# Kernel optimization log

Hardware: AMD Instinct MI355X
Metric: run time of the kernel (lower is better)

## Reference

```python
import jax, jax.numpy as jnp
import numpy as np

B, S, D, H = 2, 2048, 2048, 16
DH = D // H  # 128
EPS = 1e-6


def _rms_norm(x, w):
    # RMSNorm over last dim with learnable scale
    var = jnp.mean(jnp.square(x), axis=-1, keepdims=True)
    return x * jax.lax.rsqrt(var + EPS) * w


def _apply_rope(x, angles):
    # x: [B, S, H, DH]; angles: [S, DH//2]; interleaved pair rotation
    xs = x.reshape(*x.shape[:-1], DH // 2, 2)
    x0, x1 = xs[..., 0], xs[..., 1]
    cos = jnp.cos(angles)[None, :, None, :]  # [1,S,1,DH/2]
    sin = jnp.sin(angles)[None, :, None, :]
    r0 = x0 * cos - x1 * sin
    r1 = x0 * sin + x1 * cos
    return jnp.stack([r0, r1], axis=-1).reshape(x.shape)


def setup_inputs() -> dict:
    key = jax.random.key(0)
    ks = jax.random.split(key, 4)
    x = jax.random.normal(ks[0], (B, S, D), dtype=jnp.float32)
    # standard RoPE angle table: pos * inv_freq
    inv_freq = 1.0 / (10000.0 ** (jnp.arange(0, DH, 2, dtype=jnp.float32) / DH))
    pos = jnp.arange(S, dtype=jnp.float32)
    rp_freqs = pos[:, None] * inv_freq[None, :]  # [S, DH/2]
    Win = jax.random.normal(ks[1], (3 * D, D), dtype=jnp.float32) * (D ** -0.5)
    b_in = jnp.zeros((3 * D,), dtype=jnp.float32)
    Wout = jax.random.normal(ks[2], (D, D), dtype=jnp.float32) * (D ** -0.5)
    b_out = jnp.zeros((D,), dtype=jnp.float32)
    qk_w = jnp.ones((DH,), dtype=jnp.float32)
    out_w = jnp.ones((D,), dtype=jnp.float32)
    return {"x": x, "rp_freqs": rp_freqs, "Win": Win, "b_in": b_in,
            "Wout": Wout, "b_out": b_out, "qk_w": qk_w, "out_w": out_w}


def reference(x, rp_freqs, Win, b_in, Wout, b_out, qk_w, out_w):
    b, s, d = x.shape
    qkv = jnp.einsum('bsd,ed->bse', x, Win) + b_in  # [B,S,3D]
    qkv = qkv.reshape(b, s, 3, H, DH)
    q, k, v = qkv[:, :, 0], qkv[:, :, 1], qkv[:, :, 2]  # each [B,S,H,DH]
    q = _apply_rope(q, rp_freqs)
    k = _apply_rope(k, rp_freqs)
    q = _rms_norm(q, qk_w)
    k = _rms_norm(k, qk_w)
    # causal SDPA, scale = 1/sqrt(DH) (default)
    a = jax.nn.dot_product_attention(q, k, v, is_causal=True)  # [B,S,H,DH]
    a = a.reshape(b, s, d)
    a = _rms_norm(a, out_w)
    return jnp.einsum('bsd,ed->bse', a, Wout) + b_out
```

## Files before the change

### kernel.cpp

```cpp
#include <hip/hip_runtime.h>
#include <cstdint>
#include <cstddef>

#define Bq  2
#define Sq  2048
#define Dq  2048
#define Hq  16
#define DHq 128
#define E3q 6144

typedef __attribute__((ext_vector_type(8))) short s16x8;
typedef __attribute__((ext_vector_type(4))) float f32x4;

__device__ __forceinline__ unsigned short f2bf(float f){
  union { float f; unsigned u; } v; v.f = f;
  unsigned r = v.u + 0x7FFFu + ((v.u >> 16) & 1u);
  return (unsigned short)(r >> 16);
}
__device__ __forceinline__ float bf2f(unsigned short b){
  union { unsigned u; float f; } v; v.u = ((unsigned)b) << 16;
  return v.f;
}
__device__ __forceinline__ unsigned cvtpk_bf16(float lo, float hi){
  unsigned r;
  asm("v_cvt_pk_bf16_f32 %0, %1, %2" : "=v"(r) : "v"(lo), "v"(hi));
  return r;
}

__device__ __forceinline__ void gload_lds16(const void* g, void* l){
  __builtin_amdgcn_global_load_lds(
      (const __attribute__((address_space(1))) void*)g,
      (__attribute__((address_space(3))) void*)l, 16, 0, 0);
}

__global__ __launch_bounds__(256) void k_convert(const float* __restrict__ in,
                                                 unsigned short* __restrict__ out, int n4){
  int stride = gridDim.x * blockDim.x;
  for (int i = blockIdx.x*blockDim.x + threadIdx.x; i < n4; i += stride){
    float4 v = reinterpret_cast<const float4*>(in)[i];
    ushort4 o;
    o.x = f2bf(v.x); o.y = f2bf(v.y); o.z = f2bf(v.z); o.w = f2bf(v.w);
    reinterpret_cast<ushort4*>(out)[i] = o;
  }
}

template<int F32OUT>
__global__ __launch_bounds__(256, 2) void k_gemm_bt(const unsigned short* __restrict__ A,
                                                    const unsigned short* __restrict__ Bt,
                                                    const float* __restrict__ bias,
                                                    void* __restrict__ C,
                                                    int M, int N, int K){
  const int bid = blockIdx.x;
  const int xcd = bid & 7, u = bid >> 3;
  const int by = xcd*4 + (u & 3);
  const int bx = u >> 2;
  const int m0 = by * 128, n0 = bx * 256;

  const int tid = threadIdx.x;
  const int w = tid >> 6, lane = tid & 63, g = lane >> 4, c = lane & 15;

  __shared__ __align__(16) unsigned short L[3 * 12288];

  const int NT = K >> 5;

  const int r0 = tid >> 2, pc = tid & 3;
  const unsigned short* Ab0 = &A [(size_t)(m0 + r0      )*K + (size_t)((pc ^ (((r0      )>>1)&3))*8)];
  const unsigned short* Ab1 = &A [(size_t)(m0 + r0 +  64)*K + (size_t)((pc ^ (((r0 + 64)>>1)&3))*8)];
  const unsigned short* Bb0 = &Bt[(size_t)(n0 + r0      )*K + (size_t)((pc ^ (((r0      )>>1)&3))*8)];
  const unsigned short* Bb1 = &Bt[(size_t)(n0 + r0 +  64)*K + (size_t)((pc ^ (((r0 + 64)>>1)&3))*8)];
  const unsigned short* Bb2 = &Bt[(size_t)(n0 + r0 + 128)*K + (size_t)((pc ^ (((r0 +128)>>1)&3))*8)];
  const unsigned short* Bb3 = &Bt[(size_t)(n0 + r0 + 192)*K + (size_t)((pc ^ (((r0 +192)>>1)&3))*8)];

  auto stage = [&](int tile, int slot){
    const int kt = tile << 5;
    unsigned short* Ls = &L[slot * 12288];
    gload_lds16(Ab0 + kt, &Ls[tid*8]);
    gload_lds16(Ab1 + kt, &Ls[(tid+256)*8]);
    gload_lds16(Bb0 + kt, &Ls[4096 + tid*8]);
    gload_lds16(Bb1 + kt, &Ls[4096 + (tid+256)*8]);
    gload_lds16(Bb2 + kt, &Ls[4096 + (tid+512)*8]);
    gload_lds16(Bb3 + kt, &Ls[4096 + (tid+768)*8]);
  };

  f32x4 acc[8][4];
#pragma unroll
  for (int i=0;i<8;i++)
#pragma unroll
    for (int j=0;j<4;j++)
#pragma unroll
      for (int r=0;r<4;r++) acc[i][j][r] = 0.f;

  int aoff[8], boff[4];
#pragma unroll
  for (int mi=0;mi<8;mi++){
    int row = mi*16 + c;
    aoff[mi] = row*32 + ((g ^ ((row>>1)&3)) << 3);
  }
#pragma unroll
  for (int ni=0;ni<4;ni++){
    int row = w*64 + ni*16 + c;
    boff[ni] = 4096 + row*32 + ((g ^ ((row>>1)&3)) << 3);
  }

  stage(0,0); stage(1,1);

  int slot = 0;
  for (int t = 0; t < NT; ++t){
    if (t < NT-1) asm volatile("s_waitcnt vmcnt(6)" ::: "memory");
    else          asm volatile("s_waitcnt vmcnt(0)" ::: "memory");
    __builtin_amdgcn_s_barrier();
    __builtin_amdgcn_sched_barrier(0);
    if (t+2 < NT) stage(t+2, slot == 0 ? 2 : slot-1);

    const unsigned short* Ls = &L[slot * 12288];
    s16x8 bfr[4];
#pragma unroll
    for (int ni=0;ni<4;ni++) bfr[ni] = *(const s16x8*)&Ls[boff[ni]];
    __builtin_amdgcn_s_setprio(1);
#pragma unroll
    for (int mi=0;mi<8;mi++){
      s16x8 af = *(const s16x8*)&Ls[aoff[mi]];
#pragma unroll
      for (int ni=0;ni<4;ni++)
        acc[mi][ni] = __builtin_amdgcn_mfma_f32_16x16x32_bf16(af, bfr[ni], acc[mi][ni], 0,0,0);
    }
    __builtin_amdgcn_s_setprio(0);
    slot = (slot == 2) ? 0 : slot+1;
  }

#pragma unroll
  for (int ni=0;ni<4;ni++){
    const int col = n0 + w*64 + ni*16 + c;
    const float bv = bias[col];
#pragma unroll
    for (int mi=0;mi<8;mi++){
      const int row = m0 + mi*16 + g*4;
#pragma unroll
      for (int r=0;r<4;r++){
        float v = acc[mi][ni][r] + bv;
        if (F32OUT) ((float*)C)[(size_t)(row+r)*N + col] = v;
        else ((unsigned short*)C)[(size_t)(row+r)*N + col] = f2bf(v);
      }
    }
  }
}

__global__ __launch_bounds__(256) void k_rope_qk(const unsigned short* __restrict__ QKV,
                                                 const float* __restrict__ rp,
                                                 const float* __restrict__ qk_w,
                                                 unsigned short* __restrict__ Qp,
                                                 unsigned short* __restrict__ Kp){
  const int p = threadIdx.x;
  const int s = blockIdx.x*4 + threadIdx.y;
  const int h = blockIdx.y;
  const int b = blockIdx.z;
  const size_t n = (size_t)b*Sq + s;
  const int bh = b*Hq + h;

  float ang = rp[s*64 + p];
  float sn, cs; sincosf(ang, &sn, &cs);
  float w0 = qk_w[2*p], w1 = qk_w[2*p+1];
  const float QSCALE = 0.08838834764831845f * 1.4426950408889634f;

  {
    unsigned q01 = *(const unsigned*)&QKV[n*E3q + h*DHq + 2*p];
    float x0 = bf2f((unsigned short)(q01 & 0xFFFFu));
    float x1 = bf2f((unsigned short)(q01 >> 16));
    float r0 = x0*cs - x1*sn, r1 = x0*sn + x1*cs;
    float ss = r0*r0 + r1*r1;
#pragma unroll
    for (int m=1;m<64;m<<=1) ss += __shfl_xor(ss, m);
    float sc = rsqrtf(ss/128.f + 1e-6f) * QSCALE;
    unsigned short o0 = f2bf(r0*sc*w0), o1 = f2bf(r1*sc*w1);
    *(unsigned*)&Qp[((size_t)bh*Sq + s)*DHq + 2*p] = (unsigned)o0 | ((unsigned)o1<<16);
  }
  {
    unsigned k01 = *(const unsigned*)&QKV[n*E3q + Dq + h*DHq + 2*p];
    float x0 = bf2f((unsigned short)(k01 & 0xFFFFu));
    float x1 = bf2f((unsigned short)(k01 >> 16));
    float r0 = x0*cs - x1*sn, r1 = x0*sn + x1*cs;
    float ss = r0*r0 + r1*r1;
#pragma unroll
    for (int m=1;m<64;m<<=1) ss += __shfl_xor(ss, m);
    float sc = rsqrtf(ss/128.f + 1e-6f);
    unsigned short o0 = f2bf(r0*sc*w0), o1 = f2bf(r1*sc*w1);
    *(unsigned*)&Kp[((size_t)bh*Sq + s)*DHq + 2*p] = (unsigned)o0 | ((unsigned)o1<<16);
  }
}

__global__ __launch_bounds__(256) void k_transpose_v(const unsigned short* __restrict__ QKV,
                                                     unsigned short* __restrict__ Vt){
  const int sblk = blockIdx.x;
  const int bh = blockIdx.y;
  const int b = bh >> 4, h = bh & 15;
  const int tid = threadIdx.x;
  __shared__ unsigned short T[128][136];

  const size_t base = ((size_t)(b*Sq) + sblk*128) * E3q + 2*(size_t)Dq + h*DHq;
#pragma unroll
  for (int i=0;i<8;i++){
    int pk = tid + i*256;
    int row = pk >> 4, cc = (pk & 15) * 8;
    s16x8 v = *(const s16x8*)&QKV[base + (size_t)row*E3q + cc];
    *(s16x8*)&T[row][cc] = v;
  }
  __syncthreads();
  const int dh = tid >> 1, sh = (tid & 1) * 64;
  unsigned short buf[64];
#pragma unroll
  for (int s=0;s<64;s++) buf[s] = T[sh + s][dh];
  size_t obase = ((size_t)bh*DHq + dh)*Sq + sblk*128 + sh;
#pragma unroll
  for (int i=0;i<8;i++)
    *(s16x8*)&Vt[obase + i*8] = *(const s16x8*)&buf[i*8];
}

__global__ __launch_bounds__(256, 2) void k_attn(const unsigned short* __restrict__ Qp,
                                                 const unsigned short* __restrict__ Kp,
                                                 const unsigned short* __restrict__ Vt,
                                                 unsigned short* __restrict__ Ar){
  const int L = blockIdx.x;
  int bh, qtile;
  if (L < 256){ bh = L >> 3; qtile = 8 + (L & 7); }
  else { int Ml = L - 256; bh = Ml >> 3; qtile = 7 - (Ml & 7); }
  const int b = bh >> 4, h = bh & 15;
  const int tid = threadIdx.x;
  const int w = tid >> 6, lane = tid & 63, g = lane >> 4, c = lane & 15;
  const int r0w = qtile*128 + w*32;

  const unsigned short* Qh = Qp + (size_t)bh * Sq * DHq;
  const unsigned short* Kh = Kp + (size_t)bh * Sq * DHq;
  const unsigned short* Vh = Vt + (size_t)bh * DHq * Sq;

  __shared__ __align__(16) unsigned short Ks[2][64*128];
  __shared__ __align__(16) unsigned short Vs[2][128*64];
  __shared__ __align__(16) unsigned short Pl[4][32*64];
  unsigned short* Pw = &Pl[w][0];

  s16x8 qf[2][4];
#pragma unroll
  for (int mi=0;mi<2;mi++)
#pragma unroll
    for (int kc=0;kc<4;kc++)
      qf[mi][kc] = *(const s16x8*)&Qh[(size_t)(r0w + mi*16 + c)*DHq + kc*32 + g*8];

  f32x4 acc[2][8];
#pragma unroll
  for (int mi=0;mi<2;mi++)
#pragma unroll
    for (int dt=0;dt<8;dt++)
#pragma unroll
      for (int r=0;r<4;r++) acc[mi][dt][r] = 0.f;
  float m_r[2] = { -INFINITY, -INFINITY };
  float l_p[2] = { 0.f, 0.f };

  const int nsteps = 2*qtile + 2;

  auto stage = [&](int j0s, int bufi){
#pragma unroll
    for (int i=0;i<4;i++){
      int pk = tid + i*256;
      int row = pk>>4, pcc = pk&15;
      gload_lds16(&Kh[(size_t)(j0s+row)*DHq + ((pcc^(row&7))<<3)], &Ks[bufi][pk*8]);
    }
#pragma unroll
    for (int i=0;i<4;i++){
      int pk = tid + i*256;
      int row = pk>>3, pcc = pk&7;
      gload_lds16(&Vh[(size_t)row*Sq + j0s + ((pcc^(row&7))<<3)], &Vs[bufi][pk*8]);
    }
  };

  stage(0, 0);
  __syncthreads();

  for (int t=0; t<nsteps; ++t){
    const int j0 = t*64;
    if (t+1 < nsteps) stage((t+1)*64, (t+1)&1);

    if (j0 <= r0w + 31){
      const unsigned short* Kc = &Ks[t&1][0];
      const unsigned short* Vc = &Vs[t&1][0];

      f32x4 sv[2][4];
#pragma unroll
      for (int mi=0;mi<2;mi++)
#pragma unroll
        for (int js=0;js<4;js++)
#pragma unroll
          for (int r=0;r<4;r++) sv[mi][js][r] = 0.f;

      __builtin_amdgcn_s_setprio(1);
#pragma unroll
      for (int js=0;js<4;js++){
        s16x8 kf[4];
#pragma unroll
        for (int kc=0;kc<4;kc++)
          kf[kc] = *(const s16x8*)&Kc[(js*16 + c)*128 + (((kc*4+g)^(c&7))<<3)];
#pragma unroll
        for (int mi=0;mi<2;mi++)
#pragma unroll
          for (int kc=0;kc<4;kc++)
            sv[mi][js] = __builtin_amdgcn_mfma_f32_16x16x32_bf16(kf[kc], qf[mi][kc], sv[mi][js], 0,0,0);
      }
      __builtin_amdgcn_s_setprio(0);

      if (j0 + 63 > r0w){
#pragma unroll
        for (int mi=0;mi<2;mi++){
          const int q = r0w + mi*16 + c;
#pragma unroll
          for (int js=0;js<4;js++)
#pragma unroll
            for (int r=0;r<4;r++)
              if (j0 + js*16 + g*4 + r > q) sv[mi][js][r] = -INFINITY;
        }
      }

      float pmx[2];
#pragma unroll
      for (int mi=0;mi<2;mi++){
        float mx = fmaxf(fmaxf(sv[mi][0][0],sv[mi][0][1]), fmaxf(sv[mi][0][2],sv[mi][0][3]));
#pragma unroll
        for (int js=1;js<4;js++){
          float a = fmaxf(fmaxf(sv[mi][js][0],sv[mi][js][1]), fmaxf(sv[mi][js][2],sv[mi][js][3]));
          mx = fmaxf(mx, a);
        }
        mx = fmaxf(mx, __shfl_xor(mx, 16));
        mx = fmaxf(mx, __shfl_xor(mx, 32));
        pmx[mi] = mx;
      }
      int need = (pmx[0] > m_r[0] + 8.f) | (pmx[1] > m_r[1] + 8.f);
      if (__any(need)){
#pragma unroll
        for (int mi=0;mi<2;mi++){
          float mnew = fmaxf(m_r[mi], pmx[mi]);
          float corr = exp2f(m_r[mi] - mnew);
          l_p[mi] *= corr;
          m_r[mi] = mnew;
#pragma unroll
          for (int dt=0;dt<8;dt++)
#pragma unroll
            for (int r=0;r<4;r++) acc[mi][dt][r] *= corr;
        }
      }
#pragma unroll
      for (int mi=0;mi<2;mi++){
        const float mm = m_r[mi];
        const int rowoff = (mi*16 + c)*64;
#pragma unroll
        for (int js=0;js<4;js++){
          float e0 = exp2f(sv[mi][js][0] - mm);
          float e1 = exp2f(sv[mi][js][1] - mm);
          float e2 = exp2f(sv[mi][js][2] - mm);
          float e3 = exp2f(sv[mi][js][3] - mm);
          l_p[mi] += (e0+e1)+(e2+e3);
          uint2 pk2;
          pk2.x = cvtpk_bf16(e0, e1);
          pk2.y = cvtpk_bf16(e2, e3);
          const int kc8 = js*2 + (g>>1);
          *(uint2*)&Pw[rowoff + ((kc8 ^ (c&7))<<3) + (g&1)*4] = pk2;
        }
      }

      s16x8 pfr[2][2];
#pragma unroll
      for (int mi=0;mi<2;mi++)
#pragma unroll
        for (int kc=0;kc<2;kc++)
          pfr[mi][kc] = *(const s16x8*)&Pw[(mi*16 + c)*64 + (((kc*4+g)^(c&7))<<3)];
      __builtin_amdgcn_s_setprio(1);
#pragma unroll
      for (int dt=0; dt<8; dt++){
#pragma unroll
        for (int kc=0;kc<2;kc++){
          s16x8 vfr = *(const s16x8*)&Vc[(dt*16 + c)*64 + (((kc*4+g)^(c&7))<<3)];
#pragma unroll
          for (int mi=0;mi<2;mi++)
            acc[mi][dt] = __builtin_amdgcn_mfma_f32_16x16x32_bf16(vfr, pfr[mi][kc], acc[mi][dt], 0,0,0);
        }
      }
      __builtin_amdgcn_s_setprio(0);
    }
    __syncthreads();
  }

#pragma unroll
  for (int mi=0;mi<2;mi++){
    float l = l_p[mi];
    l += __shfl_xor(l, 16);
    l += __shfl_xor(l, 32);
    const float inv = 1.f / l;
    const int row = r0w + mi*16 + c;
    unsigned short* dst = &Ar[((size_t)(b*Sq + row))*Dq + h*DHq];
#pragma unroll
    for (int dt=0; dt<8; dt++){
      uint2 o2;
      o2.x = cvtpk_bf16(acc[mi][dt][0]*inv, acc[mi][dt][1]*inv);
      o2.y = cvtpk_bf16(acc[mi][dt][2]*inv, acc[mi][dt][3]*inv);
      *(uint2*)&dst[dt*16 + g*4] = o2;
    }
  }
}

__global__ __launch_bounds__(256) void k_rmsnorm(unsigned short* __restrict__ A,
                                                 const float* __restrict__ w){
  const int row = blockIdx.x;
  const int tid = threadIdx.x;
  s16x8 v = *(const s16x8*)&A[(size_t)row*Dq + tid*8];
  float f[8]; float ss = 0.f;
#pragma unroll
  for (int i=0;i<8;i++){ f[i] = bf2f((unsigned short)v[i]); ss += f[i]*f[i]; }
#pragma unroll
  for (int m=1;m<64;m<<=1) ss += __shfl_xor(ss, m);
  __shared__ float red[4];
  if ((tid&63)==0) red[tid>>6] = ss;
  __syncthreads();
  ss = red[0]+red[1]+red[2]+red[3];
  float sc = rsqrtf(ss/2048.f + 1e-6f);
  unsigned short o[8];
#pragma unroll
  for (int i=0;i<8;i++) o[i] = f2bf(f[i]*sc*w[tid*8+i]);
  *(s16x8*)&A[(size_t)row*Dq + tid*8] = *(const s16x8*)o;
}

extern "C" void kernel_launch(void* const* d_in, const int* in_sizes, int n_in,
                              void* d_out, int out_size, void* d_ws, size_t ws_size,
                              hipStream_t stream){
  const float* x     = (const float*)d_in[0];
  const float* rp    = (const float*)d_in[1];
  const float* Win   = (const float*)d_in[2];
  const float* b_in  = (const float*)d_in[3];
  const float* Wout  = (const float*)d_in[4];
  const float* b_out = (const float*)d_in[5];
  const float* qk_w  = (const float*)d_in[6];
  const float* out_w = (const float*)d_in[7];
  float* outp = (float*)d_out;

  if (ws_size < (160ull<<20)) return;

  char* ws = (char*)d_ws;
  unsigned short* Xb    = (unsigned short*)(ws);
  unsigned short* Wb    = (unsigned short*)(ws + (16ull<<20));
  unsigned short* Woutb = (unsigned short*)(ws + (40ull<<20));
  unsigned short* QKVb  = (unsigned short*)(ws + (48ull<<20));
  unsigned short* Qp    = (unsigned short*)(ws + (96ull<<20));
  unsigned short* Kp    = (unsigned short*)(ws + (112ull<<20));
  unsigned short* Vt    = (unsigned short*)(ws + (128ull<<20));
  unsigned short* Ar    = (unsigned short*)(ws + (144ull<<20));

  k_convert<<<2048, 256, 0, stream>>>(x,    Xb,    (Bq*Sq*Dq)/4);
  k_convert<<<2048, 256, 0, stream>>>(Win,  Wb,    (E3q*Dq)/4);
  k_convert<<<1024, 256, 0, stream>>>(Wout, Woutb, (Dq*Dq)/4);
  k_gemm_bt<0><<<768, 256, 0, stream>>>(Xb, Wb, b_in, QKVb, Bq*Sq, E3q, Dq);
  k_rope_qk<<<dim3(Sq/4, Hq, Bq), dim3(64,4), 0, stream>>>(QKVb, rp, qk_w, Qp, Kp);
  k_transpose_v<<<dim3(Sq/128, Bq*Hq), 256, 0, stream>>>(QKVb, Vt);
  k_attn<<<512, 256, 0, stream>>>(Qp, Kp, Vt, Ar);
  k_rmsnorm<<<Bq*Sq, 256, 0, stream>>>(Ar, out_w);
  k_gemm_bt<1><<<256, 256, 0, stream>>>(Ar, Woutb, b_out, outp, Bq*Sq, Dq, Dq);
}
```

Baseline: 299.7 us.

## Replace QKV projection GEMM with 8-phase pipelined 128x384 tile kernel

```diff
diff --git a/kernel.cpp b/kernel.cpp
--- a/kernel.cpp
+++ b/kernel.cpp
@@ -41,6 +41,138 @@
     ushort4 o;
     o.x = f2bf(v.x); o.y = f2bf(v.y); o.z = f2bf(v.z); o.w = f2bf(v.w);
     reinterpret_cast<ushort4*>(out)[i] = o;
+  }
+}
+
+__global__ __launch_bounds__(512, 1) void k_gemm1_8ph(const unsigned short* __restrict__ A,
+                                                      const unsigned short* __restrict__ Bt,
+                                                      const float* __restrict__ bias,
+                                                      unsigned short* __restrict__ C){
+  const int K = 2048, N = 6144;
+  const int bid = blockIdx.x;
+  const int xcd = bid & 7, u = bid >> 3;
+  const int m0 = (xcd*4 + (u & 3)) * 128;
+  const int n0 = (u >> 2) * 384;
+
+  const int tid = threadIdx.x;
+  const int lane = tid & 63, w = tid >> 6, g = lane >> 4, c = lane & 15;
+  const int wm = w >> 2, wn = w & 3;
+
+  __shared__ __align__(16) unsigned short L[65536];
+
+  const int srow = tid >> 2, spc = tid & 3;
+  const int ssw = (spc ^ ((srow >> 1) & 3)) << 3;
+  const unsigned short* aSrc  = A  + (size_t)(m0 + srow      )*K + ssw;
+  const unsigned short* bSrc0 = Bt + (size_t)(n0 + srow      )*K + ssw;
+  const unsigned short* bSrc1 = Bt + (size_t)(n0 + srow + 128)*K + ssw;
+  const unsigned short* bSrc2 = Bt + (size_t)(n0 + srow + 256)*K + ssw;
+
+  auto stA = [&](int t, int h){
+    gload_lds16(aSrc + t*64 + h*32, &L[((t&1)*2 + h)*4096 + tid*8]);
+  };
+  auto stB = [&](int t, int h, int uu){
+    const unsigned short* s = (uu==0) ? bSrc0 : (uu==1) ? bSrc1 : bSrc2;
+    gload_lds16(s + t*64 + h*32, &L[16384 + ((t&1)*2 + h)*12288 + uu*4096 + tid*8]);
+  };
+
+  int aoff[4], boff[6];
+#pragma unroll
+  for (int mf=0; mf<4; ++mf){
+    int row = wm*64 + mf*16 + c;
+    aoff[mf] = row*32 + ((g ^ ((row>>1)&3)) << 3);
+  }
+#pragma unroll
+  for (int nf=0; nf<6; ++nf){
+    int row = wn*96 + nf*16 + c;
+    boff[nf] = row*32 + ((g ^ ((row>>1)&3)) << 3);
+  }
+
+  f32x4 acc[4][6];
+#pragma unroll
+  for (int i=0;i<4;i++)
+#pragma unroll
+    for (int j=0;j<6;j++)
+#pragma unroll
+      for (int r=0;r<4;r++) acc[i][j][r] = 0.f;
+
+  auto RDA = [&](int b, int h, s16x8* af){
+    const int ab = (b*2 + h)*4096;
+#pragma unroll
+    for (int mf=0; mf<4; ++mf) af[mf] = *(const s16x8*)&L[ab + aoff[mf]];
+  };
+  auto RDB = [&](int b, int h, int nh, s16x8* bf){
+    const int bb = 16384 + (b*2 + h)*12288;
+#pragma unroll
+    for (int j=0; j<3; ++j) bf[j] = *(const s16x8*)&L[bb + boff[nh*3 + j]];
+  };
+  auto MM = [&](s16x8* af, s16x8* bf, int nh){
+    __builtin_amdgcn_s_setprio(1);
+#pragma unroll
+    for (int mf=0; mf<4; ++mf)
+#pragma unroll
+      for (int j=0; j<3; ++j)
+        acc[mf][nh*3+j] = __builtin_amdgcn_mfma_f32_16x16x32_bf16(af[mf], bf[j], acc[mf][nh*3+j], 0,0,0);
+    __builtin_amdgcn_s_setprio(0);
+  };
+  auto BAR = [&](){
+    __builtin_amdgcn_sched_barrier(0);
+    __builtin_amdgcn_s_barrier();
+    __builtin_amdgcn_sched_barrier(0);
+  };
+
+  stA(0,0); stB(0,0,0); stB(0,0,1); stB(0,0,2);
+  stA(0,1); stB(0,1,0); stB(0,1,1); stB(0,1,2);
+  stA(1,0); stB(1,0,0); stB(1,0,1); stB(1,0,2);
+  asm volatile("s_waitcnt vmcnt(4)" ::: "memory");
+  __builtin_amdgcn_s_barrier();
+
+  for (int i=0; i<16; ++i){
+    const int T0 = 2*i, T1 = 2*i + 1;
+    const bool st = (i < 15);
+    s16x8 af[4], bf[3];
+    RDA(0,0,af); RDB(0,0,0,bf);
+    stA(T1,1); stB(T1,1,0);
+    BAR(); MM(af,bf,0); BAR();
+    RDB(0,0,1,bf);
+    stB(T1,1,1); stB(T1,1,2);
+    BAR(); MM(af,bf,1); BAR();
+    RDA(0,1,af); RDB(0,1,0,bf);
+    if (st){ stA(T0+2,0); stB(T0+2,0,0); }
+    BAR(); MM(af,bf,0); BAR();
+    RDB(0,1,1,bf);
+    if (st){ stB(T0+2,0,1); stB(T0+2,0,2); }
+    __builtin_amdgcn_sched_barrier(0);
+    if (st) asm volatile("s_waitcnt vmcnt(4)" ::: "memory");
+    else    asm volatile("s_waitcnt vmcnt(0)" ::: "memory");
+    BAR(); MM(af,bf,1); BAR();
+    RDA(1,0,af); RDB(1,0,0,bf);
+    if (st){ stA(T0+2,1); stB(T0+2,1,0); }
+    BAR(); MM(af,bf,0); BAR();
+    RDB(1,0,1,bf);
+    if (st){ stB(T0+2,1,1); stB(T0+2,1,2); }
+    BAR(); MM(af,bf,1); BAR();
+    RDA(1,1,af); RDB(1,1,0,bf);
+    if (st){ stA(T1+2,0); stB(T1+2,0,0); }
+    BAR(); MM(af,bf,0); BAR();
+    RDB(1,1,1,bf);
+    if (st){ stB(T1+2,0,1); stB(T1+2,0,2); }
+    __builtin_amdgcn_sched_barrier(0);
+    if (st) asm volatile("s_waitcnt vmcnt(4)" ::: "memory");
+    else    asm volatile("s_waitcnt vmcnt(0)" ::: "memory");
+    BAR(); MM(af,bf,1); BAR();
+  }
+
+#pragma unroll
+  for (int nf=0; nf<6; ++nf){
+    const int col = n0 + wn*96 + nf*16 + c;
+    const float bv = bias[col];
+#pragma unroll
+    for (int mf=0; mf<4; ++mf){
+      const int row = m0 + wm*64 + mf*16 + g*4;
+#pragma unroll
+      for (int r=0; r<4; ++r)
+        C[(size_t)(row+r)*N + col] = f2bf(acc[mf][nf][r] + bv);
+    }
   }
 }
 
@@ -452,7 +584,7 @@
   k_convert<<<2048, 256, 0, stream>>>(x,    Xb,    (Bq*Sq*Dq)/4);
   k_convert<<<2048, 256, 0, stream>>>(Win,  Wb,    (E3q*Dq)/4);
   k_convert<<<1024, 256, 0, stream>>>(Wout, Woutb, (Dq*Dq)/4);
-  k_gemm_bt<0><<<768, 256, 0, stream>>>(Xb, Wb, b_in, QKVb, Bq*Sq, E3q, Dq);
+  k_gemm1_8ph<<<512, 512, 0, stream>>>(Xb, Wb, b_in, QKVb);
   k_rope_qk<<<dim3(Sq/4, Hq, Bq), dim3(64,4), 0, stream>>>(QKVb, rp, qk_w, Qp, Kp);
   k_transpose_v<<<dim3(Sq/128, Bq*Hq), 256, 0, stream>>>(QKVb, Vt);
   k_attn<<<512, 256, 0, stream>>>(Qp, Kp, Vt, Ar);
```

Result: faster. 288.1 us (-3.9%).

## Add 256x384-tile 8-wave QKV GEMM with triple-buffered LDS pipeline

Applied to the files above, without the earlier changes.

```diff
diff --git a/kernel.cpp b/kernel.cpp
--- a/kernel.cpp
+++ b/kernel.cpp
@@ -41,6 +41,121 @@
     ushort4 o;
     o.x = f2bf(v.x); o.y = f2bf(v.y); o.z = f2bf(v.z); o.w = f2bf(v.w);
     reinterpret_cast<ushort4*>(out)[i] = o;
+  }
+}
+
+__global__ __launch_bounds__(512, 2) void k_gemm1_8ph(const unsigned short* __restrict__ A,
+                                                      const unsigned short* __restrict__ Bt,
+                                                      const float* __restrict__ bias,
+                                                      unsigned short* __restrict__ C){
+  const int K = 2048, N = 6144, NT = 64;
+  const int bid = blockIdx.x;
+  const int xcd = bid & 7, u = bid >> 3;
+  const int m0 = (xcd*2 + (u & 1)) * 256;
+  const int n0 = (u >> 1) * 384;
+
+  const int tid = threadIdx.x;
+  const int lane = tid & 63, w = tid >> 6, g = lane >> 4, c = lane & 15;
+  const int wm = w >> 2, wn = w & 3;
+
+  __shared__ __align__(16) unsigned short L[3 * 20480];
+
+  const int srow = tid >> 2;
+  const int ssw = ((tid & 3) ^ ((srow >> 1) & 3)) * 8;
+  const unsigned short* aS0 = A  + (size_t)(m0 + srow      )*K + ssw;
+  const unsigned short* aS1 = A  + (size_t)(m0 + srow + 128)*K + ssw;
+  const unsigned short* bS0 = Bt + (size_t)(n0 + srow      )*K + ssw;
+  const unsigned short* bS1 = Bt + (size_t)(n0 + srow + 128)*K + ssw;
+  const unsigned short* bS2 = Bt + (size_t)(n0 + srow + 256)*K + ssw;
+
+  auto stX = [&](int t, int s){
+    const int kt = t*32;
+    unsigned short* Ls = &L[s*20480];
+    gload_lds16(aS0 + kt, &Ls[tid*8]);
+    gload_lds16(aS1 + kt, &Ls[4096 + tid*8]);
+    gload_lds16(bS0 + kt, &Ls[8192 + tid*8]);
+  };
+  auto stY = [&](int t, int s){
+    const int kt = t*32;
+    unsigned short* Ls = &L[s*20480];
+    gload_lds16(bS1 + kt, &Ls[12288 + tid*8]);
+    gload_lds16(bS2 + kt, &Ls[16384 + tid*8]);
+  };
+
+  int aoff[8], boff[6];
+#pragma unroll
+  for (int mf=0; mf<8; ++mf){
+    int row = wm*128 + mf*16 + c;
+    aoff[mf] = row*32 + ((g ^ ((row>>1)&3)) << 3);
+  }
+#pragma unroll
+  for (int nf=0; nf<6; ++nf){
+    int row = wn*96 + nf*16 + c;
+    boff[nf] = 8192 + row*32 + ((g ^ ((row>>1)&3)) << 3);
+  }
+
+  f32x4 acc[8][6];
+#pragma unroll
+  for (int i=0;i<8;i++)
+#pragma unroll
+    for (int j=0;j<6;j++)
+#pragma unroll
+      for (int r=0;r<4;r++) acc[i][j][r] = 0.f;
+
+  stX(0,0); stY(0,0); stX(1,1); stY(1,1);
+  asm volatile("s_waitcnt vmcnt(5)" ::: "memory");
+  __builtin_amdgcn_s_barrier();
+
+  int slot = 0;
+  for (int t = 0; t < NT; ++t){
+    const unsigned short* Ls = &L[slot * 20480];
+    const bool st = (t+2 < NT);
+    const int s2 = (slot == 0) ? 2 : slot-1;
+
+    s16x8 bf[6], af[4];
+#pragma unroll
+    for (int nf=0;nf<6;nf++) bf[nf] = *(const s16x8*)&Ls[boff[nf]];
+#pragma unroll
+    for (int mf=0;mf<4;mf++) af[mf] = *(const s16x8*)&Ls[aoff[mf]];
+    if (st) stX(t+2, s2);
+    __builtin_amdgcn_s_barrier();
+    __builtin_amdgcn_s_setprio(1);
+#pragma unroll
+    for (int mf=0;mf<4;mf++)
+#pragma unroll
+      for (int nf=0;nf<6;nf++)
+        acc[mf][nf] = __builtin_amdgcn_mfma_f32_16x16x32_bf16(af[mf], bf[nf], acc[mf][nf], 0,0,0);
+    __builtin_amdgcn_s_setprio(0);
+    __builtin_amdgcn_s_barrier();
+
+#pragma unroll
+    for (int mf=0;mf<4;mf++) af[mf] = *(const s16x8*)&Ls[aoff[4+mf]];
+    if (st) stY(t+2, s2);
+    __builtin_amdgcn_s_barrier();
+    __builtin_amdgcn_s_setprio(1);
+#pragma unroll
+    for (int mf=0;mf<4;mf++)
+#pragma unroll
+      for (int nf=0;nf<6;nf++)
+        acc[4+mf][nf] = __builtin_amdgcn_mfma_f32_16x16x32_bf16(af[mf], bf[nf], acc[4+mf][nf], 0,0,0);
+    __builtin_amdgcn_s_setprio(0);
+    if (t < NT-2) asm volatile("s_waitcnt vmcnt(5)" ::: "memory");
+    else          asm volatile("s_waitcnt vmcnt(0)" ::: "memory");
+    __builtin_amdgcn_s_barrier();
+    slot = (slot == 2) ? 0 : slot+1;
+  }
+
+#pragma unroll
+  for (int nf=0; nf<6; ++nf){
+    const int col = n0 + wn*96 + nf*16 + c;
+    const float bv = bias[col];
+#pragma unroll
+    for (int mf=0; mf<8; ++mf){
+      const int row = m0 + wm*128 + mf*16 + g*4;
+#pragma unroll
+      for (int r=0; r<4; ++r)
+        C[(size_t)(row+r)*N + col] = f2bf(acc[mf][nf][r] + bv);
+    }
   }
 }
 
@@ -452,7 +567,7 @@
   k_convert<<<2048, 256, 0, stream>>>(x,    Xb,    (Bq*Sq*Dq)/4);
   k_convert<<<2048, 256, 0, stream>>>(Win,  Wb,    (E3q*Dq)/4);
   k_convert<<<1024, 256, 0, stream>>>(Wout, Woutb, (Dq*Dq)/4);
-  k_gemm_bt<0><<<768, 256, 0, stream>>>(Xb, Wb, b_in, QKVb, Bq*Sq, E3q, Dq);
+  k_gemm1_8ph<<<256, 512, 0, stream>>>(Xb, Wb, b_in, QKVb);
   k_rope_qk<<<dim3(Sq/4, Hq, Bq), dim3(64,4), 0, stream>>>(QKVb, rp, qk_w, Qp, Kp);
   k_transpose_v<<<dim3(Sq/128, Bq*Hq), 256, 0, stream>>>(QKVb, Vt);
   k_attn<<<512, 256, 0, stream>>>(Qp, Kp, Vt, Ar);
```

Measured after the change: 284.3 us. 1.05x faster.
